# Kernel tuning notes

Measured on AMD Instinct MI355X. Metric: run time of the kernel, lower is better.

Reference implementation:

```python
import jax, jax.numpy as jnp
import numpy as np

DT = 0.1
WHEELBASE = 2.8
STATE_DIM = 12


def setup_inputs() -> dict:
    key = jax.random.key(0)
    k1, k2, k3 = jax.random.split(key, 3)
    b, l, h = 512, 64, 80
    x0 = jax.random.normal(k1, (b, STATE_DIM), dtype=jnp.float32)
    controls = jax.random.normal(k2, (b, l, h, 3), dtype=jnp.float32)
    deg = jax.random.uniform(k3, (b, 5), dtype=jnp.float32)
    return {"x0": x0, "controls": controls, "deg": deg}


def reference(x0, controls, deg):
    b, l, h, _ = controls.shape
    # degradation scales, broadcast over the l (candidate) dim: [b, 1]
    steer_scale = jnp.maximum(deg[:, 0:1], 0.05)
    brake_scale = jnp.maximum(deg[:, 1:2], 0.05)
    throttle_scale = jnp.maximum(deg[:, 2:3], 0.05)
    friction = jnp.maximum(deg[:, 4:5], 0.1)

    x_init = jnp.broadcast_to(x0[:, None, :], (b, l, x0.shape[-1]))  # [b,l,12]

    def step(x, u):  # x: [b,l,12], u: [b,l,3]
        delta = steer_scale * jnp.tanh(u[..., 0])
        fb = brake_scale * jax.nn.sigmoid(u[..., 1])
        fx = throttle_scale * jax.nn.sigmoid(u[..., 2])
        px, py, psi, vx, vy = (x[..., 0], x[..., 1], x[..., 2], x[..., 3], x[..., 4])
        speed = jnp.sqrt(vx * vx + vy * vy + 1e-06)
        acc = jnp.minimum(jnp.maximum(2.8 * fx - 6.5 * fb, -7.5 * friction), 3.0)
        speed2 = jnp.maximum(speed + acc * DT, 0.0)
        tan_d = jnp.tan(jnp.clip(delta, -0.75, 0.75))
        raw_yaw = speed2 / WHEELBASE * tan_d
        yaw_lim = jnp.maximum(friction * 9.81 / jnp.maximum(speed2, 2.0), 0.15)
        yaw_rate = jnp.clip(raw_yaw, -1.0, 1.0) * yaw_lim
        beta = jnp.clip(jnp.arctan(0.45 * tan_d), -0.65, 0.65)
        psi2 = psi + yaw_rate * DT
        vx2 = speed2 * jnp.cos(psi2 + beta)
        vy2 = speed2 * jnp.sin(psi2 + beta)
        px2 = px + vx2 * DT
        py2 = py + vy2 * DT
        ax = (vx2 - vx) / DT
        ay = (vy2 - vy) / DT
        x2 = jnp.stack([px2, py2, psi2, vx2, vy2, yaw_rate, ax, ay, beta, delta, fb, fx], -1)
        return x2, x2

    controls_t = jnp.moveaxis(controls, 2, 0)  # [h,b,l,3]
    _, traj = jax.lax.scan(step, x_init, controls_t)  # traj: [h,b,l,12]
    traj = jnp.concatenate([x_init[None], traj], axis=0)  # [h+1,b,l,12]
    return jnp.moveaxis(traj, 0, 2)  # [b,l,h+1,12]
```

## Files before the change

### kernel.cpp

```cpp
#include <hip/hip_runtime.h>
#include <math.h>


#define N_B 512
#define N_L 64
#define N_H 80
#define DT_F 0.1f
#define PITCH_F4 61
#define STEPS_PER_CHUNK 20

__device__ __forceinline__ float fast_rcp(float x) { return __builtin_amdgcn_rcpf(x); }

__device__ __forceinline__ float fast_tanh(float x) {
    const float e2 = __expf(2.0f * x);
    return (e2 - 1.0f) * fast_rcp(e2 + 1.0f);
}

__device__ __forceinline__ float fast_sigmoid(float x) {
    return fast_rcp(1.0f + __expf(-x));
}

__device__ __forceinline__ float fast_atan_small(float z) {
    const float z2 = z * z;
    float p = 1.0f / 9.0f;
    p = fmaf(p, z2, -1.0f / 7.0f);
    p = fmaf(p, z2, 1.0f / 5.0f);
    p = fmaf(p, z2, -1.0f / 3.0f);
    p = fmaf(p, z2, 1.0f);
    return z * p;
}

struct Ctl { float delta, fb, fx, tan_d, beta, acc; };

__device__ __forceinline__ Ctl make_ctl(float u0, float u1, float u2,
                                        float steer_scale, float brake_scale,
                                        float throttle_scale, float neg_brake_lim) {
    Ctl t;
    t.delta = steer_scale * fast_tanh(u0);
    t.fb = brake_scale    * fast_sigmoid(u1);
    t.fx = throttle_scale * fast_sigmoid(u2);
    const float dc = fminf(fmaxf(t.delta, -0.75f), 0.75f);
    float sd, cd;
    __sincosf(dc, &sd, &cd);
    t.tan_d = sd * fast_rcp(cd);
    t.beta = fminf(fmaxf(fast_atan_small(0.45f * t.tan_d), -0.65f), 0.65f);
    t.acc = fminf(fmaxf(2.8f * t.fx - 6.5f * t.fb, neg_brake_lim), 3.0f);
    return t;
}

__global__ __launch_bounds__(64) void degraded_bicycle_rollout_kernel(
    const float* __restrict__ x0,
    const float* __restrict__ controls,
    const float* __restrict__ deg,
    float* __restrict__ out)
{
    __shared__ float4 lds4[N_L * PITCH_F4];

    const int lane = threadIdx.x;
    const int b = blockIdx.x;
    const int tid = b * 64 + lane;

    const float* dg = deg + b * 5;
    const float steer_scale    = fmaxf(dg[0], 0.05f);
    const float brake_scale    = fmaxf(dg[1], 0.05f);
    const float throttle_scale = fmaxf(dg[2], 0.05f);
    const float friction       = fmaxf(dg[4], 0.1f);

    const float4* x0v = reinterpret_cast<const float4*>(x0 + b * 12);
    const float4 xi0 = x0v[0];
    const float4 xi1 = x0v[1];
    const float4 xi2 = x0v[2];

    {
        float4* ov = reinterpret_cast<float4*>(out + (size_t)tid * 972);
        ov[0] = xi0; ov[1] = xi1; ov[2] = xi2;
    }

    float px  = xi0.x;
    float py  = xi0.y;
    float psi = xi0.z;
    float vx  = xi0.w;
    float vy  = xi1.x;

    const float4* uc = reinterpret_cast<const float4*>(controls + (size_t)tid * 240);

    const float neg_brake_lim = -7.5f * friction;
    const float yaw_num = friction * 9.81f;
    const float inv_wheelbase = 1.0f / 2.8f;

    float4* lrow = &lds4[lane * PITCH_F4];

    float4 c0 = uc[0];
    float4 c1 = uc[1];
    float4 c2 = uc[2];

    for (int c = 0; c < 4; ++c) {
        #pragma unroll
        for (int gg = 0; gg < 5; ++gg) {
            const int g = c * 5 + gg;
            float4 n0 = c0, n1 = c1, n2 = c2;
            if (g < 19) {
                n0 = uc[(g + 1) * 3 + 0];
                n1 = uc[(g + 1) * 3 + 1];
                n2 = uc[(g + 1) * 3 + 2];
            }

            const Ctl tA = make_ctl(c0.x, c0.y, c0.z, steer_scale, brake_scale, throttle_scale, neg_brake_lim);
            const Ctl tB = make_ctl(c0.w, c1.x, c1.y, steer_scale, brake_scale, throttle_scale, neg_brake_lim);
            const Ctl tC = make_ctl(c1.z, c1.w, c2.x, steer_scale, brake_scale, throttle_scale, neg_brake_lim);
            const Ctl tD = make_ctl(c2.y, c2.z, c2.w, steer_scale, brake_scale, throttle_scale, neg_brake_lim);

#define ROLL_STEP(T, RR)                                                          \
            {                                                                     \
                const float speed  = __builtin_amdgcn_sqrtf(fmaf(vx, vx, fmaf(vy, vy, 1e-6f))); \
                const float speed2 = fmaxf(fmaf((T).acc, DT_F, speed), 0.0f);     \
                const float raw_yaw = speed2 * inv_wheelbase * (T).tan_d;         \
                const float yaw_lim = fmaxf(yaw_num * fast_rcp(fmaxf(speed2, 2.0f)), 0.15f); \
                const float yaw_rate = fminf(fmaxf(raw_yaw, -1.0f), 1.0f) * yaw_lim; \
                const float psi2 = fmaf(yaw_rate, DT_F, psi);                     \
                float s_, c_;                                                     \
                __sincosf(psi2 + (T).beta, &s_, &c_);                             \
                const float vx2 = speed2 * c_;                                    \
                const float vy2 = speed2 * s_;                                    \
                const float px2 = fmaf(vx2, DT_F, px);                            \
                const float py2 = fmaf(vy2, DT_F, py);                            \
                const float ax = (vx2 - vx) * 10.0f;                              \
                const float ay = (vy2 - vy) * 10.0f;                              \
                lrow[(RR) * 3 + 0] = make_float4(px2, py2, psi2, vx2);            \
                lrow[(RR) * 3 + 1] = make_float4(vy2, yaw_rate, ax, ay);          \
                lrow[(RR) * 3 + 2] = make_float4((T).beta, (T).delta, (T).fb, (T).fx); \
                px = px2; py = py2; psi = psi2; vx = vx2; vy = vy2;               \
            }

            ROLL_STEP(tA, gg * 4 + 0)
            ROLL_STEP(tB, gg * 4 + 1)
            ROLL_STEP(tC, gg * 4 + 2)
            ROLL_STEP(tD, gg * 4 + 3)
#undef ROLL_STEP

            c0 = n0; c1 = n1; c2 = n2;
        }

        const size_t out_chunk = (size_t)b * 62208 + 12 + c * 240;
        #pragma unroll 10
        for (int i = 0; i < 60; ++i) {
            const int flat = i * 64 + lane;
            const int l = flat / 60;
            const int q = flat - l * 60;
            const float4 v = lds4[l * PITCH_F4 + q];
            *reinterpret_cast<float4*>(out + out_chunk + (size_t)l * 972 + q * 4) = v;
        }
    }
}

extern "C" void kernel_launch(void* const* d_in, const int* in_sizes, int n_in,
                              void* d_out, int out_size, void* d_ws, size_t ws_size,
                              hipStream_t stream) {
    (void)in_sizes; (void)n_in; (void)d_ws; (void)ws_size; (void)out_size;
    const float* x0       = (const float*)d_in[0];
    const float* controls = (const float*)d_in[1];
    const float* deg      = (const float*)d_in[2];
    float* out            = (float*)d_out;

    dim3 grid(N_B), block(64);
    hipLaunchKernelGGL(degraded_bicycle_rollout_kernel, grid, block, 0, stream,
                       x0, controls, deg, out);
}
```

Baseline: 39.82 us.

## Double-buffer LDS staging and interleave output flushes with rollout compute

Splits the 80-step rollout into 10 chunks of 8 steps with two LDS buffers, so the previous chunk's output is flushed to global memory in two slices interleaved with computing the next chunk. This aims to overlap the scattered global stores with the serial per-lane dynamics instead of stalling after each chunk. LDS footprint per block shrinks (2x25 vs 61 float4 per row), which could raise occupancy. The kernel has no explicit barriers, relying on the single-wavefront block for LDS visibility, and adds more flush loop overhead.

Measured after the change: 35.43 us. 11.0% less time.

```diff
diff --git a/kernel.cpp b/kernel.cpp
--- a/kernel.cpp
+++ b/kernel.cpp
@@ -6,8 +6,9 @@
 #define N_L 64
 #define N_H 80
 #define DT_F 0.1f
-#define PITCH_F4 61
-#define STEPS_PER_CHUNK 20
+#define PITCH_F4 25
+#define SPC 8
+#define NCH 10
 
 __device__ __forceinline__ float fast_rcp(float x) { return __builtin_amdgcn_rcpf(x); }
 
@@ -54,7 +55,7 @@
     const float* __restrict__ deg,
     float* __restrict__ out)
 {
-    __shared__ float4 lds4[N_L * PITCH_F4];
+    __shared__ float4 lds4[2][N_L * PITCH_F4];
 
     const int lane = threadIdx.x;
     const int b = blockIdx.x;
@@ -88,16 +89,32 @@
     const float yaw_num = friction * 9.81f;
     const float inv_wheelbase = 1.0f / 2.8f;
 
-    float4* lrow = &lds4[lane * PITCH_F4];
+    const size_t out_b = (size_t)b * 62208 + 12;
+
+#define FLUSH_SLICE(FBUF, FC, I0, I1)                                             \
+    {                                                                             \
+        const size_t obase = out_b + (size_t)(FC) * (SPC * 12);                   \
+        _Pragma("unroll")                                                         \
+        for (int i = (I0); i < (I1); ++i) {                                       \
+            const unsigned flat = i * 64 + lane;                                  \
+            const unsigned l = flat / 24u;                                        \
+            const unsigned q = flat - l * 24u;                                    \
+            const float4 v = lds4[FBUF][l * PITCH_F4 + q];                        \
+            *reinterpret_cast<float4*>(out + obase + (size_t)l * 972 + q * 4) = v;\
+        }                                                                         \
+    }
 
     float4 c0 = uc[0];
     float4 c1 = uc[1];
     float4 c2 = uc[2];
 
-    for (int c = 0; c < 4; ++c) {
+    for (int c = 0; c < NCH; ++c) {
+        const int cur = c & 1;
+        float4* lrow = &lds4[cur][lane * PITCH_F4];
+
         #pragma unroll
-        for (int gg = 0; gg < 5; ++gg) {
-            const int g = c * 5 + gg;
+        for (int gg = 0; gg < 2; ++gg) {
+            const int g = c * 2 + gg;
             float4 n0 = c0, n1 = c1, n2 = c2;
             if (g < 19) {
                 n0 = uc[(g + 1) * 3 + 0];
@@ -139,18 +156,16 @@
 #undef ROLL_STEP
 
             c0 = n0; c1 = n1; c2 = n2;
-        }
 
-        const size_t out_chunk = (size_t)b * 62208 + 12 + c * 240;
-        #pragma unroll 10
-        for (int i = 0; i < 60; ++i) {
-            const int flat = i * 64 + lane;
-            const int l = flat / 60;
-            const int q = flat - l * 60;
-            const float4 v = lds4[l * PITCH_F4 + q];
-            *reinterpret_cast<float4*>(out + out_chunk + (size_t)l * 972 + q * 4) = v;
+            if (c > 0) {
+                if (gg == 0) FLUSH_SLICE(cur ^ 1, c - 1, 0, 12)
+                else         FLUSH_SLICE(cur ^ 1, c - 1, 12, 24)
+            }
         }
     }
+
+    FLUSH_SLICE((NCH - 1) & 1, NCH - 1, 0, 24)
+#undef FLUSH_SLICE
 }
 
 extern "C" void kernel_launch(void* const* d_in, const int* in_sizes, int n_in,
```
